# Optimization experiments

Measured on AMD Instinct MI355X. Metric: run time of the kernel, lower is better.

Reference implementation:

```python
import jax, jax.numpy as jnp
import numpy as np

N = 30000      # nodes
E = 480000     # edges (before self loops)
NFEAT = 128
H = 16         # heads
C = 32         # per-head channels = nhid
NCLASS = 10
G = 64         # graphs in batch
ATT_SLOPE = 0.2   # GATv2Conv negative_slope default
ACT_SLOPE = 0.01  # F.leaky_relu default


def setup_inputs() -> dict:
    key = jax.random.key(0)
    ks = jax.random.split(key, 16)
    def glorot(k, shape):
        fan = sum(shape[:2]) if len(shape) > 1 else shape[0]
        return jax.random.normal(k, shape, jnp.float32) * (2.0 / fan) ** 0.5
    inp = {
        "x": jax.random.normal(ks[0], (N, NFEAT), jnp.float32),
        # layer 1: lin_l / lin_r map NFEAT -> H*C, attention vector att [H, C]
        "Wl1": glorot(ks[1], (NFEAT, H * C)), "bl1": jnp.zeros((H * C,), jnp.float32),
        "Wr1": glorot(ks[2], (NFEAT, H * C)), "br1": jnp.zeros((H * C,), jnp.float32),
        "att1": glorot(ks[3], (H, C)), "b1": jnp.zeros((C,), jnp.float32),
        # layer 2: nhid(=C) -> H*C
        "Wl2": glorot(ks[4], (C, H * C)), "bl2": jnp.zeros((H * C,), jnp.float32),
        "Wr2": glorot(ks[5], (C, H * C)), "br2": jnp.zeros((H * C,), jnp.float32),
        "att2": glorot(ks[6], (H, C)), "b2": jnp.zeros((C,), jnp.float32),
        # classifier nhid -> nclass
        "Wc": glorot(ks[7], (C, NCLASS)), "bc": jnp.zeros((NCLASS,), jnp.float32),
        "edge_index": jax.random.randint(ks[8], (2, E), 0, N, jnp.int32),
        "batch": jnp.sort(jax.random.randint(ks[9], (N,), 0, G, jnp.int32)),
    }
    return inp


def _gatv2_layer(x, Wl, bl, Wr, br, att, b, src, dst, n):
    # GATv2Conv, concat=False (mean over heads), eval mode (no dropout)
    xl = (x @ Wl + bl).reshape(n, H, C)   # messages (x_j)
    xr = (x @ Wr + br).reshape(n, H, C)   # query side (x_i)
    e = jax.nn.leaky_relu(xl[src] + xr[dst], ATT_SLOPE)      # [E', H, C]
    score = jnp.einsum('ehc,hc->eh', e, att)                 # [E', H]
    # segment softmax over incoming edges of each dst node
    m = jax.ops.segment_max(score, dst, num_segments=n)
    ex = jnp.exp(score - m[dst])
    denom = jax.ops.segment_sum(ex, dst, num_segments=n)
    alpha = ex / denom[dst]                                  # [E', H]
    out = jax.ops.segment_sum(alpha[:, :, None] * xl[src], dst, num_segments=n)
    return out.mean(axis=1) + b                              # [n, C]


def reference(x, Wl1, bl1, Wr1, br1, att1, b1, Wl2, bl2, Wr2, br2, att2, b2, Wc, bc, edge_index, batch):
    # add self loops (PyG GATv2Conv default add_self_loops=True)
    loop = jnp.arange(N, dtype=edge_index.dtype)
    src = jnp.concatenate([edge_index[0], loop])
    dst = jnp.concatenate([edge_index[1], loop])

    h = jax.nn.leaky_relu(_gatv2_layer(x, Wl1, bl1, Wr1, br1, att1, b1, src, dst, N), ACT_SLOPE)
    h = jax.nn.leaky_relu(_gatv2_layer(h, Wl2, bl2, Wr2, br2, att2, b2, src, dst, N), ACT_SLOPE)
    # dropout is identity in eval mode
    # global mean pool over graphs
    summed = jax.ops.segment_sum(h, batch, num_segments=G)               # [G, C]
    counts = jax.ops.segment_sum(jnp.ones((N,), h.dtype), batch, num_segments=G)
    pooled = summed / jnp.maximum(counts, 1.0)[:, None]
    logits = pooled @ Wc + bc
    return logits / 1.0  # temperature = 1.0
```

## Files before the change

### kernel.cpp

```cpp
#include <hip/hip_runtime.h>
#include <float.h>

#define NNODES 30000
#define NEDGES 480000
#define NFEATK 128
#define NH 16
#define NC 32
#define HC 512
#define NCLASSES 10
#define NG 64
#define CAP 96

using half2v = __attribute__((ext_vector_type(2))) _Float16;
using half4 = __attribute__((ext_vector_type(4))) _Float16;
using half8 = __attribute__((ext_vector_type(8))) _Float16;
using f32x4 = __attribute__((ext_vector_type(4))) float;

__global__ void prep0_kernel(const float* __restrict__ x, _Float16* __restrict__ xh,
                             const float* __restrict__ Wl1, const float* __restrict__ Wr1,
                             _Float16* __restrict__ Wlt1, _Float16* __restrict__ Wrt1,
                             const float* __restrict__ Wl2, const float* __restrict__ Wr2,
                             _Float16* __restrict__ Wlt2, _Float16* __restrict__ Wrt2,
                             int* __restrict__ cnt, int* __restrict__ csr) {
    int gtid = blockIdx.x * blockDim.x + threadIdx.x;
    int gstride = gridDim.x * blockDim.x;
    for (int i = gtid; i < NNODES * NFEATK / 4; i += gstride) {
        float4 v = *(const float4*)&x[i * 4];
        half4 h = {(_Float16)v.x, (_Float16)v.y, (_Float16)v.z, (_Float16)v.w};
        *(half4*)&xh[i * 4] = h;
    }
    for (int i = gtid; i < 2 * 512 * NFEATK; i += gstride) {
        int sel = i >= 512 * NFEATK;
        int idx = i - sel * 512 * NFEATK;
        const float* W = sel ? Wr1 : Wl1;
        _Float16* Wt = sel ? Wrt1 : Wlt1;
        int n = idx & 511, k = idx >> 9;
        Wt[n * NFEATK + k] = (_Float16)W[idx];
    }
    for (int i = gtid; i < 2 * 512 * NC; i += gstride) {
        int sel = i >= 512 * NC;
        int idx = i - sel * 512 * NC;
        const float* W = sel ? Wr2 : Wl2;
        _Float16* Wt = sel ? Wrt2 : Wlt2;
        int n = idx & 511, k = idx >> 9;
        Wt[n * NC + k] = (_Float16)W[idx];
    }
    for (int i = gtid; i < NNODES; i += gstride) {
        cnt[i] = 1;
        csr[i * CAP] = i;
    }
}

__global__ void scatter_kernel(const int* __restrict__ src, const int* __restrict__ dst,
                               int* __restrict__ cnt, int* __restrict__ csr) {
    int e = blockIdx.x * blockDim.x + threadIdx.x;
    if (e >= NEDGES) return;
    int s = src[e], d = dst[e];
    int pos = atomicAdd(&cnt[d], 1);
    csr[d * CAP + pos] = s;
}

template <int K>
__launch_bounds__(256)
__global__ void dual_gemm_kernel(const _Float16* __restrict__ A,
                                 const _Float16* __restrict__ Wlt, const _Float16* __restrict__ Wrt,
                                 const float* __restrict__ bl, const float* __restrict__ br,
                                 _Float16* __restrict__ Yl, _Float16* __restrict__ Yr) {
    constexpr int Kc = K / 8;
    constexpr int AH = 64 * K;
    constexpr int BH = 128 * K;
    constexpr int YSH = 64 * 136;
    constexpr int SMEMH = (AH + BH > YSH) ? (AH + BH) : YSH;
    __shared__ __align__(16) _Float16 smem[SMEMH];
    _Float16* as = smem;
    _Float16* bs = smem + AH;

    int tid = threadIdx.x;
    int sel = blockIdx.y >> 2;
    int nbase = (blockIdx.y & 3) * 128;
    const _Float16* Bt = sel ? Wrt : Wlt;
    const float* bias = sel ? br : bl;
    _Float16* Y = sel ? Yr : Yl;
    int mb = blockIdx.x;

    for (int c = tid; c < 64 * Kc; c += 256) {
        int row = c / Kc, k8 = c % Kc;
        int arow = mb * 64 + row; if (arow > NNODES - 1) arow = NNODES - 1;
        half8 v = *(const half8*)&A[(size_t)arow * K + k8 * 8];
        *(half8*)&as[(row * Kc + (k8 ^ (row & (Kc - 1)))) * 8] = v;
    }
    for (int c = tid; c < 128 * Kc; c += 256) {
        int row = c / Kc, k8 = c % Kc;
        half8 v = *(const half8*)&Bt[(size_t)(nbase + row) * K + k8 * 8];
        *(half8*)&bs[(row * Kc + (k8 ^ (row & (Kc - 1)))) * 8] = v;
    }
    __syncthreads();

    int wave = tid >> 6, lane = tid & 63;
    int quad = lane >> 4, l16 = lane & 15;
    int am = l16 & (Kc - 1);

    f32x4 acc[8];
    #pragma unroll
    for (int f = 0; f < 8; f++) acc[f] = (f32x4){0.f, 0.f, 0.f, 0.f};

    #pragma unroll
    for (int kk = 0; kk < Kc; kk += 4) {
        int k8 = (kk + quad) ^ am;
        half8 a = *(const half8*)&as[((wave * 16 + l16) * Kc + k8) * 8];
        #pragma unroll
        for (int f = 0; f < 8; f++) {
            half8 b = *(const half8*)&bs[((f * 16 + l16) * Kc + k8) * 8];
            acc[f] = __builtin_amdgcn_mfma_f32_16x16x32_f16(a, b, acc[f], 0, 0, 0);
        }
    }
    __syncthreads();

    _Float16* ys = smem;
    #pragma unroll
    for (int f = 0; f < 8; f++) {
        float bv = bias[nbase + f * 16 + l16];
        #pragma unroll
        for (int r = 0; r < 4; r++) {
            ys[(wave * 16 + quad * 4 + r) * 136 + f * 16 + l16] = (_Float16)(acc[f][r] + bv);
        }
    }
    __syncthreads();
    int mtop = mb * 64;
    for (int c = tid; c < 64 * 16; c += 256) {
        int r = c >> 4, cc = (c & 15) * 8;
        int grow = mtop + r;
        if (grow < NNODES)
            *(half8*)&Y[(size_t)grow * HC + nbase + cc] = *(half8*)&ys[r * 136 + cc];
    }
}

__device__ inline half2v lrelu2(half2v e) {
    half2v s = e * half2v{(_Float16)0.2f, (_Float16)0.2f};
    return __builtin_elementwise_max(e, s);
}

#if __has_builtin(__builtin_amdgcn_fdot2)
#define FDOT2(a, b, c) __builtin_amdgcn_fdot2((a), (b), (c), false)
#else
__device__ inline float fdot2_sw(half2v a, half2v b, float c) {
    half2v p = a * b;
    return c + (float)p.x + (float)p.y;
}
#define FDOT2(a, b, c) fdot2_sw((a), (b), (c))
#endif

template <typename OUT>
__launch_bounds__(256)
__global__ void gat_edge_kernel(const _Float16* __restrict__ xlh, const _Float16* __restrict__ xrh,
                                const float* __restrict__ att, const float* __restrict__ bvec,
                                const int* __restrict__ cnt, const int* __restrict__ csr_src,
                                OUT* __restrict__ hout) {
    int wv = threadIdx.x >> 6;
    int t = threadIdx.x & 63;
    int d = blockIdx.x * 4 + wv;
    int col = t * 8;

    half8 xrq = *(const half8*)&xrh[(size_t)d * HC + col];
    half2v xr0 = {xrq[0], xrq[1]}, xr1 = {xrq[2], xrq[3]};
    half2v xr2 = {xrq[4], xrq[5]}, xr3 = {xrq[6], xrq[7]};
    float4 atta = *(const float4*)&att[col];
    float4 attb = *(const float4*)&att[col + 4];
    half2v at0 = {(_Float16)atta.x, (_Float16)atta.y};
    half2v at1 = {(_Float16)atta.z, (_Float16)atta.w};
    half2v at2 = {(_Float16)attb.x, (_Float16)attb.y};
    half2v at3 = {(_Float16)attb.z, (_Float16)attb.w};

    int beg = d * CAP, end = beg + cnt[d];

    float l = 0.f;
    float a[8];
    #pragma unroll
    for (int c = 0; c < 8; c++) a[c] = 0.f;

    for (int i = beg; i < end; i += 4) {
        int n = end - i;
        int s0 = csr_src[i];
        int s1 = csr_src[n > 1 ? i + 1 : i];
        int s2 = csr_src[n > 2 ? i + 2 : i];
        int s3 = csr_src[n > 3 ? i + 3 : i];
        half8 q0 = *(const half8*)&xlh[(size_t)s0 * HC + col];
        half8 q1 = *(const half8*)&xlh[(size_t)s1 * HC + col];
        half8 q2 = *(const half8*)&xlh[(size_t)s2 * HC + col];
        half8 q3 = *(const half8*)&xlh[(size_t)s3 * HC + col];

        float v0 = 0.f, v1 = 0.f, v2 = 0.f, v3 = 0.f;
        v0 = FDOT2(lrelu2(half2v{q0[0], q0[1]} + xr0), at0, v0);
        v0 = FDOT2(lrelu2(half2v{q0[2], q0[3]} + xr1), at1, v0);
        v0 = FDOT2(lrelu2(half2v{q0[4], q0[5]} + xr2), at2, v0);
        v0 = FDOT2(lrelu2(half2v{q0[6], q0[7]} + xr3), at3, v0);
        v1 = FDOT2(lrelu2(half2v{q1[0], q1[1]} + xr0), at0, v1);
        v1 = FDOT2(lrelu2(half2v{q1[2], q1[3]} + xr1), at1, v1);
        v1 = FDOT2(lrelu2(half2v{q1[4], q1[5]} + xr2), at2, v1);
        v1 = FDOT2(lrelu2(half2v{q1[6], q1[7]} + xr3), at3, v1);
        v2 = FDOT2(lrelu2(half2v{q2[0], q2[1]} + xr0), at0, v2);
        v2 = FDOT2(lrelu2(half2v{q2[2], q2[3]} + xr1), at1, v2);
        v2 = FDOT2(lrelu2(half2v{q2[4], q2[5]} + xr2), at2, v2);
        v2 = FDOT2(lrelu2(half2v{q2[6], q2[7]} + xr3), at3, v2);
        v3 = FDOT2(lrelu2(half2v{q3[0], q3[1]} + xr0), at0, v3);
        v3 = FDOT2(lrelu2(half2v{q3[2], q3[3]} + xr1), at1, v3);
        v3 = FDOT2(lrelu2(half2v{q3[4], q3[5]} + xr2), at2, v3);
        v3 = FDOT2(lrelu2(half2v{q3[6], q3[7]} + xr3), at3, v3);

        v0 += __shfl_xor(v0, 1); v1 += __shfl_xor(v1, 1);
        v2 += __shfl_xor(v2, 1); v3 += __shfl_xor(v3, 1);
        v0 += __shfl_xor(v0, 2); v1 += __shfl_xor(v1, 2);
        v2 += __shfl_xor(v2, 2); v3 += __shfl_xor(v3, 2);

        float p0 = __expf(v0);
        float p1 = (n > 1) ? __expf(v1) : 0.f;
        float p2 = (n > 2) ? __expf(v2) : 0.f;
        float p3 = (n > 3) ? __expf(v3) : 0.f;
        l += (p0 + p1) + (p2 + p3);

        #pragma unroll
        for (int c = 0; c < 8; c++) {
            a[c] += p0 * (float)q0[c];
            a[c] += p1 * (float)q1[c];
            a[c] += p2 * (float)q2[c];
            a[c] += p3 * (float)q3[c];
        }
    }

    float inv = 1.0f / l;
    #pragma unroll
    for (int c = 0; c < 8; c++) a[c] *= inv;

    #pragma unroll
    for (int off = 4; off < 64; off <<= 1) {
        #pragma unroll
        for (int c = 0; c < 8; c++) a[c] += __shfl_xor(a[c], off);
    }

    if (t < 4) {
        #pragma unroll
        for (int c = 0; c < 8; c++) {
            float r = a[c] * (1.0f / (float)NH) + bvec[t * 8 + c];
            r = (r > 0.f) ? r : 0.01f * r;
            hout[(size_t)d * NC + t * 8 + c] = (OUT)r;
        }
    }
}

__launch_bounds__(1024)
__global__ void pool_classify_kernel(const float* __restrict__ h, const int* __restrict__ batch,
                                     const float* __restrict__ Wc, const float* __restrict__ bc,
                                     float* __restrict__ out) {
    int g = blockIdx.x;
    int lo = 0, hi = NNODES;
    while (lo < hi) { int mid = (lo + hi) >> 1; if (batch[mid] < g) lo = mid + 1; else hi = mid; }
    int start = lo;
    hi = NNODES;
    while (lo < hi) { int mid = (lo + hi) >> 1; if (batch[mid] <= g) lo = mid + 1; else hi = mid; }
    int endn = lo;
    int cntg = endn - start;

    int tid = threadIdx.x;
    int c = tid & 31, nl = tid >> 5;
    float s = 0.f;
    for (int n = start + nl; n < endn; n += 32) s += h[n * NC + c];
    __shared__ float red[1024];
    red[tid] = s;
    __syncthreads();
    if (tid < 32) {
        float t = 0.f;
        #pragma unroll
        for (int j = 0; j < 32; j++) t += red[j * 32 + tid];
        red[tid] = t / fmaxf((float)cntg, 1.0f);
    }
    __syncthreads();
    if (tid < NCLASSES) {
        float sum = bc[tid];
        #pragma unroll
        for (int cc = 0; cc < NC; cc++) sum += red[cc] * Wc[cc * NCLASSES + tid];
        out[g * NCLASSES + tid] = sum;
    }
}


extern "C" void kernel_launch(void* const* d_in, const int* in_sizes, int n_in,
                              void* d_out, int out_size, void* d_ws, size_t ws_size,
                              hipStream_t stream) {
    const float* x    = (const float*)d_in[0];
    const float* Wl1  = (const float*)d_in[1];
    const float* bl1  = (const float*)d_in[2];
    const float* Wr1  = (const float*)d_in[3];
    const float* br1  = (const float*)d_in[4];
    const float* att1 = (const float*)d_in[5];
    const float* b1   = (const float*)d_in[6];
    const float* Wl2  = (const float*)d_in[7];
    const float* bl2  = (const float*)d_in[8];
    const float* Wr2  = (const float*)d_in[9];
    const float* br2  = (const float*)d_in[10];
    const float* att2 = (const float*)d_in[11];
    const float* b2   = (const float*)d_in[12];
    const float* Wc   = (const float*)d_in[13];
    const float* bc   = (const float*)d_in[14];
    const int* ei     = (const int*)d_in[15];
    const int* batch  = (const int*)d_in[16];
    float* out = (float*)d_out;

    const int* srcp = ei;
    const int* dstp = ei + NEDGES;

    char* ws = (char*)d_ws;
    size_t off = 0;
    auto alloc = [&](size_t bytes) -> void* {
        void* p = ws + off;
        off += (bytes + 255) & ~(size_t)255;
        return p;
    };
    _Float16* xlh  = (_Float16*)alloc(sizeof(_Float16) * (size_t)NNODES * HC);
    _Float16* xrh  = (_Float16*)alloc(sizeof(_Float16) * (size_t)NNODES * HC);
    _Float16* xh   = (_Float16*)alloc(sizeof(_Float16) * (size_t)NNODES * NFEATK);
    _Float16* h1   = (_Float16*)alloc(sizeof(_Float16) * (size_t)NNODES * NC);
    float* h2      = (float*)alloc(sizeof(float) * (size_t)NNODES * NC);
    _Float16* Wlt1 = (_Float16*)alloc(sizeof(_Float16) * 512 * NFEATK);
    _Float16* Wrt1 = (_Float16*)alloc(sizeof(_Float16) * 512 * NFEATK);
    _Float16* Wlt2 = (_Float16*)alloc(sizeof(_Float16) * 512 * NC);
    _Float16* Wrt2 = (_Float16*)alloc(sizeof(_Float16) * 512 * NC);
    int*   cnt     = (int*)alloc(sizeof(int) * NNODES);
    int*   csr     = (int*)alloc(sizeof(int) * (size_t)NNODES * CAP);

    prep0_kernel<<<512, 256, 0, stream>>>(x, xh, Wl1, Wr1, Wlt1, Wrt1,
                                          Wl2, Wr2, Wlt2, Wrt2, cnt, csr);
    scatter_kernel<<<(NEDGES + 255) / 256, 256, 0, stream>>>(srcp, dstp, cnt, csr);

    const int MB = (NNODES + 63) / 64;

    dual_gemm_kernel<NFEATK><<<dim3(MB, 8), 256, 0, stream>>>(xh, Wlt1, Wrt1, bl1, br1, xlh, xrh);
    gat_edge_kernel<_Float16><<<NNODES / 4, 256, 0, stream>>>(xlh, xrh, att1, b1, cnt, csr, h1);

    dual_gemm_kernel<NC><<<dim3(MB, 8), 256, 0, stream>>>(h1, Wlt2, Wrt2, bl2, br2, xlh, xrh);
    gat_edge_kernel<float><<<NNODES / 4, 256, 0, stream>>>(xlh, xrh, att2, b2, cnt, csr, h2);

    pool_classify_kernel<<<NG, 1024, 0, stream>>>(h2, batch, Wc, bc, out);
}
```

Baseline: 321.0 us.

## Use 16-bit CSR indices, K-split GEMM staging, swapped grid order, 32-bit offsets

Stores CSR source indices as unsigned short, which halves index traffic and footprint. This relies on the node count (30000) fitting in 16 bits. The dual GEMM now stages K in chunks of at most 64, cutting shared memory per block to allow higher occupancy, at the cost of an extra sync. The grid is transposed so the eight column tiles of one row block run next to each other and share the A tile in cache. Gather address arithmetic uses 32-bit unsigned offsets instead of size_t to reduce 64-bit integer math.

```diff
diff --git a/kernel.cpp b/kernel.cpp
--- a/kernel.cpp
+++ b/kernel.cpp
@@ -21,7 +21,7 @@
                              _Float16* __restrict__ Wlt1, _Float16* __restrict__ Wrt1,
                              const float* __restrict__ Wl2, const float* __restrict__ Wr2,
                              _Float16* __restrict__ Wlt2, _Float16* __restrict__ Wrt2,
-                             int* __restrict__ cnt, int* __restrict__ csr) {
+                             int* __restrict__ cnt, unsigned short* __restrict__ csr) {
     int gtid = blockIdx.x * blockDim.x + threadIdx.x;
     int gstride = gridDim.x * blockDim.x;
     for (int i = gtid; i < NNODES * NFEATK / 4; i += gstride) {
@@ -47,17 +47,17 @@
     }
     for (int i = gtid; i < NNODES; i += gstride) {
         cnt[i] = 1;
-        csr[i * CAP] = i;
+        csr[i * CAP] = (unsigned short)i;
     }
 }
 
 __global__ void scatter_kernel(const int* __restrict__ src, const int* __restrict__ dst,
-                               int* __restrict__ cnt, int* __restrict__ csr) {
+                               int* __restrict__ cnt, unsigned short* __restrict__ csr) {
     int e = blockIdx.x * blockDim.x + threadIdx.x;
     if (e >= NEDGES) return;
     int s = src[e], d = dst[e];
     int pos = atomicAdd(&cnt[d], 1);
-    csr[d * CAP + pos] = s;
+    csr[d * CAP + pos] = (unsigned short)s;
 }
 
 template <int K>
@@ -66,9 +66,10 @@
                                  const _Float16* __restrict__ Wlt, const _Float16* __restrict__ Wrt,
                                  const float* __restrict__ bl, const float* __restrict__ br,
                                  _Float16* __restrict__ Yl, _Float16* __restrict__ Yr) {
-    constexpr int Kc = K / 8;
-    constexpr int AH = 64 * K;
-    constexpr int BH = 128 * K;
+    constexpr int KS = (K > 64) ? 64 : K;
+    constexpr int KcS = KS / 8;
+    constexpr int AH = 64 * KS;
+    constexpr int BH = 128 * KS;
     constexpr int YSH = 64 * 136;
     constexpr int SMEMH = (AH + BH > YSH) ? (AH + BH) : YSH;
     __shared__ __align__(16) _Float16 smem[SMEMH];
@@ -76,42 +77,46 @@
     _Float16* bs = smem + AH;
 
     int tid = threadIdx.x;
-    int sel = blockIdx.y >> 2;
-    int nbase = (blockIdx.y & 3) * 128;
+    int sel = blockIdx.x >> 2;
+    int nbase = (blockIdx.x & 3) * 128;
     const _Float16* Bt = sel ? Wrt : Wlt;
     const float* bias = sel ? br : bl;
     _Float16* Y = sel ? Yr : Yl;
-    int mb = blockIdx.x;
-
-    for (int c = tid; c < 64 * Kc; c += 256) {
-        int row = c / Kc, k8 = c % Kc;
-        int arow = mb * 64 + row; if (arow > NNODES - 1) arow = NNODES - 1;
-        half8 v = *(const half8*)&A[(size_t)arow * K + k8 * 8];
-        *(half8*)&as[(row * Kc + (k8 ^ (row & (Kc - 1)))) * 8] = v;
-    }
-    for (int c = tid; c < 128 * Kc; c += 256) {
-        int row = c / Kc, k8 = c % Kc;
-        half8 v = *(const half8*)&Bt[(size_t)(nbase + row) * K + k8 * 8];
-        *(half8*)&bs[(row * Kc + (k8 ^ (row & (Kc - 1)))) * 8] = v;
-    }
-    __syncthreads();
+    int mb = blockIdx.y;
 
     int wave = tid >> 6, lane = tid & 63;
     int quad = lane >> 4, l16 = lane & 15;
-    int am = l16 & (Kc - 1);
+    int am = l16 & (KcS - 1);
 
     f32x4 acc[8];
     #pragma unroll
     for (int f = 0; f < 8; f++) acc[f] = (f32x4){0.f, 0.f, 0.f, 0.f};
 
     #pragma unroll
-    for (int kk = 0; kk < Kc; kk += 4) {
-        int k8 = (kk + quad) ^ am;
-        half8 a = *(const half8*)&as[((wave * 16 + l16) * Kc + k8) * 8];
-        #pragma unroll
-        for (int f = 0; f < 8; f++) {
-            half8 b = *(const half8*)&bs[((f * 16 + l16) * Kc + k8) * 8];
-            acc[f] = __builtin_amdgcn_mfma_f32_16x16x32_f16(a, b, acc[f], 0, 0, 0);
+    for (int ko = 0; ko < K / KS; ++ko) {
+        if (ko) __syncthreads();
+        for (int c = tid; c < 64 * KcS; c += 256) {
+            int row = c / KcS, k8 = c % KcS;
+            int arow = mb * 64 + row; if (arow > NNODES - 1) arow = NNODES - 1;
+            half8 v = *(const half8*)&A[(size_t)arow * K + (ko * KcS + k8) * 8];
+            *(half8*)&as[(row * KcS + (k8 ^ (row & (KcS - 1)))) * 8] = v;
+        }
+        for (int c = tid; c < 128 * KcS; c += 256) {
+            int row = c / KcS, k8 = c % KcS;
+            half8 v = *(const half8*)&Bt[(size_t)(nbase + row) * K + (ko * KcS + k8) * 8];
+            *(half8*)&bs[(row * KcS + (k8 ^ (row & (KcS - 1)))) * 8] = v;
+        }
+        __syncthreads();
+
+        #pragma unroll
+        for (int kk = 0; kk < KcS; kk += 4) {
+            int k8 = (kk + quad) ^ am;
+            half8 a = *(const half8*)&as[((wave * 16 + l16) * KcS + k8) * 8];
+            #pragma unroll
+            for (int f = 0; f < 8; f++) {
+                half8 b = *(const half8*)&bs[((f * 16 + l16) * KcS + k8) * 8];
+                acc[f] = __builtin_amdgcn_mfma_f32_16x16x32_f16(a, b, acc[f], 0, 0, 0);
+            }
         }
     }
     __syncthreads();
@@ -154,14 +159,14 @@
 __launch_bounds__(256)
 __global__ void gat_edge_kernel(const _Float16* __restrict__ xlh, const _Float16* __restrict__ xrh,
                                 const float* __restrict__ att, const float* __restrict__ bvec,
-                                const int* __restrict__ cnt, const int* __restrict__ csr_src,
+                                const int* __restrict__ cnt, const unsigned short* __restrict__ csr_src,
                                 OUT* __restrict__ hout) {
     int wv = threadIdx.x >> 6;
     int t = threadIdx.x & 63;
     int d = blockIdx.x * 4 + wv;
     int col = t * 8;
 
-    half8 xrq = *(const half8*)&xrh[(size_t)d * HC + col];
+    half8 xrq = *(const half8*)&xrh[(unsigned)d * HC + col];
     half2v xr0 = {xrq[0], xrq[1]}, xr1 = {xrq[2], xrq[3]};
     half2v xr2 = {xrq[4], xrq[5]}, xr3 = {xrq[6], xrq[7]};
     float4 atta = *(const float4*)&att[col];
@@ -184,10 +189,10 @@
         int s1 = csr_src[n > 1 ? i + 1 : i];
         int s2 = csr_src[n > 2 ? i + 2 : i];
         int s3 = csr_src[n > 3 ? i + 3 : i];
-        half8 q0 = *(const half8*)&xlh[(size_t)s0 * HC + col];
-        half8 q1 = *(const half8*)&xlh[(size_t)s1 * HC + col];
-        half8 q2 = *(const half8*)&xlh[(size_t)s2 * HC + col];
-        half8 q3 = *(const half8*)&xlh[(size_t)s3 * HC + col];
+        half8 q0 = *(const half8*)&xlh[(unsigned)s0 * HC + col];
+        half8 q1 = *(const half8*)&xlh[(unsigned)s1 * HC + col];
+        half8 q2 = *(const half8*)&xlh[(unsigned)s2 * HC + col];
+        half8 q3 = *(const half8*)&xlh[(unsigned)s3 * HC + col];
 
         float v0 = 0.f, v1 = 0.f, v2 = 0.f, v3 = 0.f;
         v0 = FDOT2(lrelu2(half2v{q0[0], q0[1]} + xr0), at0, v0);
@@ -325,7 +330,7 @@
     _Float16* Wlt2 = (_Float16*)alloc(sizeof(_Float16) * 512 * NC);
     _Float16* Wrt2 = (_Float16*)alloc(sizeof(_Float16) * 512 * NC);
     int*   cnt     = (int*)alloc(sizeof(int) * NNODES);
-    int*   csr     = (int*)alloc(sizeof(int) * (size_t)NNODES * CAP);
+    unsigned short* csr = (unsigned short*)alloc(sizeof(unsigned short) * (size_t)NNODES * CAP);
 
     prep0_kernel<<<512, 256, 0, stream>>>(x, xh, Wl1, Wr1, Wlt1, Wrt1,
                                           Wl2, Wr2, Wlt2, Wrt2, cnt, csr);
@@ -333,10 +338,10 @@
 
     const int MB = (NNODES + 63) / 64;
 
-    dual_gemm_kernel<NFEATK><<<dim3(MB, 8), 256, 0, stream>>>(xh, Wlt1, Wrt1, bl1, br1, xlh, xrh);
+    dual_gemm_kernel<NFEATK><<<dim3(8, MB), 256, 0, stream>>>(xh, Wlt1, Wrt1, bl1, br1, xlh, xrh);
     gat_edge_kernel<_Float16><<<NNODES / 4, 256, 0, stream>>>(xlh, xrh, att1, b1, cnt, csr, h1);
 
-    dual_gemm_kernel<NC><<<dim3(MB, 8), 256, 0, stream>>>(h1, Wlt2, Wrt2, bl2, br2, xlh, xrh);
+    dual_gemm_kernel<NC><<<dim3(8, MB), 256, 0, stream>>>(h1, Wlt2, Wrt2, bl2, br2, xlh, xrh);
     gat_edge_kernel<float><<<NNODES / 4, 256, 0, stream>>>(xlh, xrh, att2, b2, cnt, csr, h2);
 
     pool_classify_kernel<<<NG, 1024, 0, stream>>>(h2, batch, Wc, bc, out);
```

After: 319.8 us. No clear change (-0.4%).
